# Kernel tuning notes

Hardware: AMD Instinct MI355X
Metric: run time of the kernel (lower is better)

Reference implementation:

```python
import jax, jax.numpy as jnp
import numpy as np

N, E = 50000, 800000
D_IN, D_H, D_OUT = 128, 128, 128


def setup_inputs() -> dict:
    key = jax.random.key(0)
    ks = jax.random.split(key, 8)
    x = jax.random.normal(ks[0], (N, D_IN), dtype=jnp.float32)
    edge_index = jax.random.randint(ks[1], (2, E), 0, N, dtype=jnp.int64)
    s_in = 1.0 / np.sqrt(D_IN)
    s_h = 1.0 / np.sqrt(D_H)
    W1 = jax.random.normal(ks[2], (D_IN, D_H), dtype=jnp.float32) * s_in
    b1 = jnp.zeros((D_H,), jnp.float32)
    Wg = jax.random.normal(ks[3], (D_H, D_H), dtype=jnp.float32) * s_h
    bg = jnp.zeros((D_H,), jnp.float32)
    W2 = jax.random.normal(ks[4], (D_H, D_OUT), dtype=jnp.float32) * s_h
    b2 = jnp.zeros((D_OUT,), jnp.float32)
    return {"x": x, "edge_index": edge_index, "W1": W1, "b1": b1,
            "Wg": Wg, "bg": bg, "W2": W2, "b2": b2}


def reference(x, edge_index, W1, b1, Wg, bg, W2, b2):
    # Linear -> ReLU
    h = jax.nn.relu(x @ W1 + b1)                      # [N, D_H]
    # GCNConv: transform, add self-loops, sym-normalize, scatter-aggregate
    h = h @ Wg                                        # [N, D_H]
    row, col = edge_index[0], edge_index[1]
    loop = jnp.arange(N, dtype=edge_index.dtype)
    row = jnp.concatenate([row, loop])                # [E+N] sources
    col = jnp.concatenate([col, loop])                # [E+N] targets
    deg = jax.ops.segment_sum(jnp.ones(E + N, h.dtype), col, num_segments=N)
    dinv = jnp.where(deg > 0, jax.lax.rsqrt(deg), 0.0)
    norm = dinv[row] * dinv[col]                      # [E+N]
    agg = jax.ops.segment_sum(h[row] * norm[:, None], col, num_segments=N)
    agg = agg + bg                                    # GCNConv bias
    # ReLU -> Linear
    return jax.nn.relu(agg) @ W2 + b2                 # [N, D_OUT]
```

## Files before the change

### kernel.cpp

```cpp
#include <hip/hip_runtime.h>

#define D 128

typedef short bf16x8 __attribute__((ext_vector_type(8)));
typedef float f32x4 __attribute__((ext_vector_type(4)));

static __device__ __forceinline__ unsigned int f2bf(float f) {
  unsigned int u = __float_as_uint(f);
  return (u + 0x7FFFu + ((u >> 16) & 1u)) >> 16;
}
static __device__ __forceinline__ unsigned int pack2bf(float lo, float hi) {
  return f2bf(lo) | (f2bf(hi) << 16);
}
static __device__ __forceinline__ float bf_lo(unsigned int v) {
  return __uint_as_float(v << 16);
}
static __device__ __forceinline__ float bf_hi(unsigned int v) {
  return __uint_as_float(v & 0xFFFF0000u);
}


__global__ __launch_bounds__(256) void k_prep(const float* __restrict__ W1,
                                              const float* __restrict__ Wg,
                                              const float* __restrict__ W2,
                                              unsigned short* __restrict__ WT,
                                              int* __restrict__ deg, int N) {
  if (blockIdx.x < 3) {
    const float* W = (blockIdx.x == 0) ? W1 : (blockIdx.x == 1) ? Wg : W2;
    unsigned short* T = WT + blockIdx.x * 16384;
    for (int idx = threadIdx.x; idx < 16384; idx += 256) {
      int k = idx >> 7, j = idx & 127;
      T[j * 128 + k] = (unsigned short)f2bf(W[idx]);
    }
  } else {
    int i = (blockIdx.x - 3) * 256 + threadIdx.x;
    if (i < N) deg[i] = 0;
  }
}


#define FILL_CHUNK 2048

__global__ __launch_bounds__(256) void k_fill(const int* __restrict__ ei, int E,
                                              int* __restrict__ deg,
                                              unsigned short* __restrict__ csr16,
                                              int cap) {
  const int p = blockIdx.x & 7;
  const int base = (blockIdx.x >> 3) * FILL_CHUNK;
  const int t = threadIdx.x;
  int c[8];
#pragma unroll
  for (int u = 0; u < 8; ++u) {
    int e = base + u * 256 + t;
    c[u] = (e < E) ? ei[E + e] : -1;
  }
#pragma unroll
  for (int u = 0; u < 8; ++u) {
    if (c[u] >= 0 && (c[u] & 7) == p) {
      int e = base + u * 256 + t;
      int r = ei[e];
      int pos = atomicAdd(&deg[c[u]], 1);
      if (pos < cap)
        csr16[(size_t)c[u] * cap + pos] = (unsigned short)r;
    }
  }
}


__global__ __launch_bounds__(256) void k_mlp(const float* __restrict__ x,
                                             const unsigned short* __restrict__ W1T,
                                             const float* __restrict__ b1,
                                             const unsigned short* __restrict__ WgT,
                                             const int* __restrict__ deg,
                                             unsigned short* __restrict__ h2, int N) {
  __shared__ unsigned short xs[64][136];
  __shared__ unsigned short wB[128][136];
  const int t = threadIdx.x;
  const int wave = t >> 6, lane = t & 63;
  const int rowBase = blockIdx.x * 64;
  const int ar = lane & 15, kg = lane >> 4;

#pragma unroll
  for (int i = 0; i < 8; ++i) {
    int idx = t + i * 256;
    int r = idx >> 5, c4 = (idx & 31) << 2;
    float4 v = make_float4(0.f, 0.f, 0.f, 0.f);
    int gr = rowBase + r;
    if (gr < N) v = *(const float4*)(x + (size_t)gr * D + c4);
    *(unsigned int*)&xs[r][c4]     = pack2bf(v.x, v.y);
    *(unsigned int*)&xs[r][c4 + 2] = pack2bf(v.z, v.w);
  }
#pragma unroll
  for (int i = 0; i < 8; ++i) {
    int idx = t + i * 256;
    int r = idx >> 4, c8 = (idx & 15) << 3;
    *(uint4*)&wB[r][c8] = *(const uint4*)(W1T + r * 128 + c8);
  }
  __syncthreads();

  float bias1[8];
#pragma unroll
  for (int cf = 0; cf < 8; ++cf) bias1[cf] = b1[cf * 16 + ar];
  float dnv[4];
#pragma unroll
  for (int reg = 0; reg < 4; ++reg) {
    int gr = rowBase + wave * 16 + 4 * kg + reg;
    dnv[reg] = (gr < N) ? rsqrtf((float)(deg[gr] + 1)) : 0.f;
  }

  f32x4 acc[8];
#pragma unroll
  for (int cf = 0; cf < 8; ++cf) acc[cf] = (f32x4){0.f, 0.f, 0.f, 0.f};
#pragma unroll
  for (int ks = 0; ks < 4; ++ks) {
    bf16x8 a = *(const bf16x8*)&xs[wave * 16 + ar][ks * 32 + kg * 8];
#pragma unroll
    for (int cf = 0; cf < 8; ++cf) {
      bf16x8 b = *(const bf16x8*)&wB[cf * 16 + ar][ks * 32 + kg * 8];
      acc[cf] = __builtin_amdgcn_mfma_f32_16x16x32_bf16(a, b, acc[cf], 0, 0, 0);
    }
  }

#pragma unroll
  for (int cf = 0; cf < 8; ++cf)
#pragma unroll
    for (int reg = 0; reg < 4; ++reg) {
      float v = fmaxf(acc[cf][reg] + bias1[cf], 0.f);
      xs[wave * 16 + 4 * kg + reg][cf * 16 + ar] = (unsigned short)f2bf(v);
    }
  __syncthreads();

#pragma unroll
  for (int i = 0; i < 8; ++i) {
    int idx = t + i * 256;
    int r = idx >> 4, c8 = (idx & 15) << 3;
    *(uint4*)&wB[r][c8] = *(const uint4*)(WgT + r * 128 + c8);
  }
  __syncthreads();

#pragma unroll
  for (int cf = 0; cf < 8; ++cf) acc[cf] = (f32x4){0.f, 0.f, 0.f, 0.f};
#pragma unroll
  for (int ks = 0; ks < 4; ++ks) {
    bf16x8 a = *(const bf16x8*)&xs[wave * 16 + ar][ks * 32 + kg * 8];
#pragma unroll
    for (int cf = 0; cf < 8; ++cf) {
      bf16x8 b = *(const bf16x8*)&wB[cf * 16 + ar][ks * 32 + kg * 8];
      acc[cf] = __builtin_amdgcn_mfma_f32_16x16x32_bf16(a, b, acc[cf], 0, 0, 0);
    }
  }

#pragma unroll
  for (int cf = 0; cf < 8; ++cf)
#pragma unroll
    for (int reg = 0; reg < 4; ++reg) {
      int gr = rowBase + wave * 16 + 4 * kg + reg;
      if (gr < N)
        h2[(size_t)gr * D + cf * 16 + ar] = (unsigned short)f2bf(acc[cf][reg] * dnv[reg]);
    }
}


__global__ __launch_bounds__(256) void k_agg(const unsigned short* __restrict__ h2,
                                             const int* __restrict__ deg,
                                             const unsigned short* __restrict__ csr16,
                                             const float* __restrict__ bg,
                                             float* __restrict__ agg, int N, int cap) {
  int wave = threadIdx.x >> 6;
  int lane = threadIdx.x & 63;
  int n = blockIdx.x * 4 + wave;
  if (n >= N) return;
  const unsigned int* h2v = (const unsigned int*)h2;
  unsigned int vself = h2v[(size_t)n * 64 + lane];
  int dg = deg[n];
  float2 bgv = ((const float2*)bg)[lane];
  float dn = rsqrtf((float)(dg + 1));
  float ax = 0.f, ay = 0.f;
  int cnt = min(dg, cap);
  size_t base = (size_t)n * cap;
  int i = 0;
  for (; i + 16 <= cnt; i += 16) {
    uint4 pa = *(const uint4*)(csr16 + base + i);
    uint4 pb = *(const uint4*)(csr16 + base + i + 8);
    int s[16] = {(int)(pa.x & 0xFFFFu), (int)(pa.x >> 16),
                 (int)(pa.y & 0xFFFFu), (int)(pa.y >> 16),
                 (int)(pa.z & 0xFFFFu), (int)(pa.z >> 16),
                 (int)(pa.w & 0xFFFFu), (int)(pa.w >> 16),
                 (int)(pb.x & 0xFFFFu), (int)(pb.x >> 16),
                 (int)(pb.y & 0xFFFFu), (int)(pb.y >> 16),
                 (int)(pb.z & 0xFFFFu), (int)(pb.z >> 16),
                 (int)(pb.w & 0xFFFFu), (int)(pb.w >> 16)};
    unsigned int v[16];
#pragma unroll
    for (int u = 0; u < 16; ++u) v[u] = h2v[(size_t)s[u] * 64 + lane];
#pragma unroll
    for (int u = 0; u < 16; ++u) { ax += bf_lo(v[u]); ay += bf_hi(v[u]); }
  }
  for (; i + 8 <= cnt; i += 8) {
    uint4 pk = *(const uint4*)(csr16 + base + i);
    int s[8] = {(int)(pk.x & 0xFFFFu), (int)(pk.x >> 16),
                (int)(pk.y & 0xFFFFu), (int)(pk.y >> 16),
                (int)(pk.z & 0xFFFFu), (int)(pk.z >> 16),
                (int)(pk.w & 0xFFFFu), (int)(pk.w >> 16)};
    unsigned int v[8];
#pragma unroll
    for (int u = 0; u < 8; ++u) v[u] = h2v[(size_t)s[u] * 64 + lane];
#pragma unroll
    for (int u = 0; u < 8; ++u) { ax += bf_lo(v[u]); ay += bf_hi(v[u]); }
  }
  for (; i < cnt; ++i) {
    int s = csr16[base + i];
    unsigned int v = h2v[(size_t)s * 64 + lane];
    ax += bf_lo(v); ay += bf_hi(v);
  }
  ax += bf_lo(vself); ay += bf_hi(vself);
  float2 o;
  o.x = fmaxf(fmaf(ax, dn, bgv.x), 0.f);
  o.y = fmaxf(fmaf(ay, dn, bgv.y), 0.f);
  ((float2*)agg)[(size_t)n * 64 + lane] = o;
}


__global__ __launch_bounds__(256) void k_out(const float* __restrict__ a,
                                             const unsigned short* __restrict__ W2T,
                                             const float* __restrict__ b2,
                                             float* __restrict__ out, int N) {
  __shared__ unsigned short xs[64][136];
  __shared__ unsigned short wB[128][136];
  const int t = threadIdx.x;
  const int wave = t >> 6, lane = t & 63;
  const int rowBase = blockIdx.x * 64;
  const int ar = lane & 15, kg = lane >> 4;

#pragma unroll
  for (int i = 0; i < 8; ++i) {
    int idx = t + i * 256;
    int r = idx >> 5, c4 = (idx & 31) << 2;
    float4 v = make_float4(0.f, 0.f, 0.f, 0.f);
    int gr = rowBase + r;
    if (gr < N) v = *(const float4*)(a + (size_t)gr * D + c4);
    *(unsigned int*)&xs[r][c4]     = pack2bf(v.x, v.y);
    *(unsigned int*)&xs[r][c4 + 2] = pack2bf(v.z, v.w);
  }
#pragma unroll
  for (int i = 0; i < 8; ++i) {
    int idx = t + i * 256;
    int r = idx >> 4, c8 = (idx & 15) << 3;
    *(uint4*)&wB[r][c8] = *(const uint4*)(W2T + r * 128 + c8);
  }
  __syncthreads();

  float bias2[8];
#pragma unroll
  for (int cf = 0; cf < 8; ++cf) bias2[cf] = b2[cf * 16 + ar];

  f32x4 acc[8];
#pragma unroll
  for (int cf = 0; cf < 8; ++cf) acc[cf] = (f32x4){0.f, 0.f, 0.f, 0.f};
#pragma unroll
  for (int ks = 0; ks < 4; ++ks) {
    bf16x8 a8 = *(const bf16x8*)&xs[wave * 16 + ar][ks * 32 + kg * 8];
#pragma unroll
    for (int cf = 0; cf < 8; ++cf) {
      bf16x8 b8 = *(const bf16x8*)&wB[cf * 16 + ar][ks * 32 + kg * 8];
      acc[cf] = __builtin_amdgcn_mfma_f32_16x16x32_bf16(a8, b8, acc[cf], 0, 0, 0);
    }
  }

#pragma unroll
  for (int cf = 0; cf < 8; ++cf)
#pragma unroll
    for (int reg = 0; reg < 4; ++reg) {
      int gr = rowBase + wave * 16 + 4 * kg + reg;
      if (gr < N)
        out[(size_t)gr * D + cf * 16 + ar] = acc[cf][reg] + bias2[cf];
    }
}


extern "C" void kernel_launch(void* const* d_in, const int* in_sizes, int n_in,
                              void* d_out, int out_size, void* d_ws, size_t ws_size,
                              hipStream_t stream) {
  const float* x  = (const float*)d_in[0];
  const int*   ei = (const int*)d_in[1];
  const float* W1 = (const float*)d_in[2];
  const float* b1 = (const float*)d_in[3];
  const float* Wg = (const float*)d_in[4];
  const float* bg = (const float*)d_in[5];
  const float* W2 = (const float*)d_in[6];
  const float* b2 = (const float*)d_in[7];
  const int N = in_sizes[0] / D;
  const int E = in_sizes[1] / 2;
  float* out = (float*)d_out;

  unsigned short* h2 = (unsigned short*)d_ws;
  unsigned short* WT = h2 + (size_t)N * D;
  int*   deg  = (int*)(WT + 3 * 16384);
  unsigned short* csr16 = (unsigned short*)(deg + N);

  size_t fixed = (size_t)N * D * 2 + 3 * 16384 * 2 + (size_t)N * 4;
  int cap;
  if (ws_size >= fixed + (size_t)N * 64 * 2)      cap = 64;
  else if (ws_size >= fixed + (size_t)N * 48 * 2) cap = 48;
  else return;

  const int nzb = (N + 255) / 256;
  const int fillb = ((E + FILL_CHUNK - 1) / FILL_CHUNK) * 8;

  k_prep<<<3 + nzb, 256, 0, stream>>>(W1, Wg, W2, WT, deg, N);
  k_fill<<<fillb, 256, 0, stream>>>(ei, E, deg, csr16, cap);
  k_mlp <<<(N + 63) / 64, 256, 0, stream>>>(x, WT, b1, WT + 16384, deg, h2, N);
  k_agg <<<(N + 3) / 4, 256, 0, stream>>>(h2, deg, csr16, bg, out, N, cap);
  k_out <<<(N + 63) / 64, 256, 0, stream>>>(out, WT + 2 * 16384, b2, out, N);
}
```

Measured before the change: 131.6 us.

## Aggregate with half-wave per node and store bf16 intermediate for output GEMM

```diff
diff --git a/kernel.cpp b/kernel.cpp
--- a/kernel.cpp
+++ b/kernel.cpp
@@ -165,17 +165,17 @@
                                              const int* __restrict__ deg,
                                              const unsigned short* __restrict__ csr16,
                                              const float* __restrict__ bg,
-                                             float* __restrict__ agg, int N, int cap) {
-  int wave = threadIdx.x >> 6;
-  int lane = threadIdx.x & 63;
-  int n = blockIdx.x * 4 + wave;
+                                             unsigned short* __restrict__ h3, int N, int cap) {
+  const int half = threadIdx.x >> 5;
+  const int hl = threadIdx.x & 31;
+  const int n = blockIdx.x * 8 + half;
   if (n >= N) return;
-  const unsigned int* h2v = (const unsigned int*)h2;
-  unsigned int vself = h2v[(size_t)n * 64 + lane];
+  const uint2* h2v = (const uint2*)h2;
+  uint2 vself = h2v[(size_t)n * 32 + hl];
   int dg = deg[n];
-  float2 bgv = ((const float2*)bg)[lane];
+  float4 bgv = ((const float4*)bg)[hl];
   float dn = rsqrtf((float)(dg + 1));
-  float ax = 0.f, ay = 0.f;
+  float a0 = 0.f, a1 = 0.f, a2 = 0.f, a3 = 0.f;
   int cnt = min(dg, cap);
   size_t base = (size_t)n * cap;
   int i = 0;
@@ -190,11 +190,14 @@
                  (int)(pb.y & 0xFFFFu), (int)(pb.y >> 16),
                  (int)(pb.z & 0xFFFFu), (int)(pb.z >> 16),
                  (int)(pb.w & 0xFFFFu), (int)(pb.w >> 16)};
-    unsigned int v[16];
-#pragma unroll
-    for (int u = 0; u < 16; ++u) v[u] = h2v[(size_t)s[u] * 64 + lane];
-#pragma unroll
-    for (int u = 0; u < 16; ++u) { ax += bf_lo(v[u]); ay += bf_hi(v[u]); }
+    uint2 v[16];
+#pragma unroll
+    for (int u = 0; u < 16; ++u) v[u] = h2v[(size_t)s[u] * 32 + hl];
+#pragma unroll
+    for (int u = 0; u < 16; ++u) {
+      a0 += bf_lo(v[u].x); a1 += bf_hi(v[u].x);
+      a2 += bf_lo(v[u].y); a3 += bf_hi(v[u].y);
+    }
   }
   for (; i + 8 <= cnt; i += 8) {
     uint4 pk = *(const uint4*)(csr16 + base + i);
@@ -202,26 +205,35 @@
                 (int)(pk.y & 0xFFFFu), (int)(pk.y >> 16),
                 (int)(pk.z & 0xFFFFu), (int)(pk.z >> 16),
                 (int)(pk.w & 0xFFFFu), (int)(pk.w >> 16)};
-    unsigned int v[8];
-#pragma unroll
-    for (int u = 0; u < 8; ++u) v[u] = h2v[(size_t)s[u] * 64 + lane];
-#pragma unroll
-    for (int u = 0; u < 8; ++u) { ax += bf_lo(v[u]); ay += bf_hi(v[u]); }
+    uint2 v[8];
+#pragma unroll
+    for (int u = 0; u < 8; ++u) v[u] = h2v[(size_t)s[u] * 32 + hl];
+#pragma unroll
+    for (int u = 0; u < 8; ++u) {
+      a0 += bf_lo(v[u].x); a1 += bf_hi(v[u].x);
+      a2 += bf_lo(v[u].y); a3 += bf_hi(v[u].y);
+    }
   }
   for (; i < cnt; ++i) {
     int s = csr16[base + i];
-    unsigned int v = h2v[(size_t)s * 64 + lane];
-    ax += bf_lo(v); ay += bf_hi(v);
-  }
-  ax += bf_lo(vself); ay += bf_hi(vself);
-  float2 o;
-  o.x = fmaxf(fmaf(ax, dn, bgv.x), 0.f);
-  o.y = fmaxf(fmaf(ay, dn, bgv.y), 0.f);
-  ((float2*)agg)[(size_t)n * 64 + lane] = o;
-}
-
-
-__global__ __launch_bounds__(256) void k_out(const float* __restrict__ a,
+    uint2 v = h2v[(size_t)s * 32 + hl];
+    a0 += bf_lo(v.x); a1 += bf_hi(v.x);
+    a2 += bf_lo(v.y); a3 += bf_hi(v.y);
+  }
+  a0 += bf_lo(vself.x); a1 += bf_hi(vself.x);
+  a2 += bf_lo(vself.y); a3 += bf_hi(vself.y);
+  float r0 = fmaxf(fmaf(a0, dn, bgv.x), 0.f);
+  float r1 = fmaxf(fmaf(a1, dn, bgv.y), 0.f);
+  float r2 = fmaxf(fmaf(a2, dn, bgv.z), 0.f);
+  float r3 = fmaxf(fmaf(a3, dn, bgv.w), 0.f);
+  uint2 o;
+  o.x = pack2bf(r0, r1);
+  o.y = pack2bf(r2, r3);
+  ((uint2*)h3)[(size_t)n * 32 + hl] = o;
+}
+
+
+__global__ __launch_bounds__(256) void k_out(const unsigned short* __restrict__ h3,
                                              const unsigned short* __restrict__ W2T,
                                              const float* __restrict__ b2,
                                              float* __restrict__ out, int N) {
@@ -233,14 +245,13 @@
   const int ar = lane & 15, kg = lane >> 4;
 
 #pragma unroll
-  for (int i = 0; i < 8; ++i) {
-    int idx = t + i * 256;
-    int r = idx >> 5, c4 = (idx & 31) << 2;
-    float4 v = make_float4(0.f, 0.f, 0.f, 0.f);
+  for (int i = 0; i < 4; ++i) {
+    int idx = t + i * 256;
+    int r = idx >> 4, c8 = (idx & 15) << 3;
+    uint4 v = make_uint4(0u, 0u, 0u, 0u);
     int gr = rowBase + r;
-    if (gr < N) v = *(const float4*)(a + (size_t)gr * D + c4);
-    *(unsigned int*)&xs[r][c4]     = pack2bf(v.x, v.y);
-    *(unsigned int*)&xs[r][c4 + 2] = pack2bf(v.z, v.w);
+    if (gr < N) v = *(const uint4*)(h3 + (size_t)gr * D + c8);
+    *(uint4*)&xs[r][c8] = v;
   }
 #pragma unroll
   for (int i = 0; i < 8; ++i) {
@@ -294,11 +305,12 @@
   float* out = (float*)d_out;
 
   unsigned short* h2 = (unsigned short*)d_ws;
-  unsigned short* WT = h2 + (size_t)N * D;
+  unsigned short* h3 = h2 + (size_t)N * D;
+  unsigned short* WT = h3 + (size_t)N * D;
   int*   deg  = (int*)(WT + 3 * 16384);
   unsigned short* csr16 = (unsigned short*)(deg + N);
 
-  size_t fixed = (size_t)N * D * 2 + 3 * 16384 * 2 + (size_t)N * 4;
+  size_t fixed = (size_t)N * D * 4 + 3 * 16384 * 2 + (size_t)N * 4;
   int cap;
   if (ws_size >= fixed + (size_t)N * 64 * 2)      cap = 64;
   else if (ws_size >= fixed + (size_t)N * 48 * 2) cap = 48;
@@ -310,6 +322,6 @@
   k_prep<<<3 + nzb, 256, 0, stream>>>(W1, Wg, W2, WT, deg, N);
   k_fill<<<fillb, 256, 0, stream>>>(ei, E, deg, csr16, cap);
   k_mlp <<<(N + 63) / 64, 256, 0, stream>>>(x, WT, b1, WT + 16384, deg, h2, N);
-  k_agg <<<(N + 3) / 4, 256, 0, stream>>>(h2, deg, csr16, bg, out, N, cap);
-  k_out <<<(N + 63) / 64, 256, 0, stream>>>(out, WT + 2 * 16384, b2, out, N);
-}
+  k_agg <<<(N + 7) / 8, 256, 0, stream>>>(h2, deg, csr16, bg, h3, N, cap);
+  k_out <<<(N + 63) / 64, 256, 0, stream>>>(h3, WT + 2 * 16384, b2, out, N);
+}
```

New measurement: 125.8 us. -4.4%, faster.
